# Performance work log

Measured on AMD Instinct MI355X. Metric: run time of the kernel, lower is better.

Reference implementation:

```python
import jax, jax.numpy as jnp
import numpy as np

B, T, E, H = 4, 8192, 1024, 16
D = E // H
SCALE = 1.0 / np.sqrt(D).astype(np.float32)
EPS_FM = 1e-6
EPS_Z = 1e-8


def setup_inputs() -> dict:
    key = jax.random.key(0)
    ks = jax.random.split(key, 11)
    s = 1.0 / np.sqrt(E).astype(np.float32)  # small init so feature map stays sane
    return {
        'query': jax.random.normal(ks[0], (B, T, E), jnp.float32),
        'key': jax.random.normal(ks[1], (B, T, E), jnp.float32),
        'value': jax.random.normal(ks[2], (B, T, E), jnp.float32),
        'Wq': jax.random.normal(ks[3], (E, E), jnp.float32) * s,
        'bq': jax.random.normal(ks[4], (E,), jnp.float32) * 0.01,
        'Wk': jax.random.normal(ks[5], (E, E), jnp.float32) * s,
        'bk': jax.random.normal(ks[6], (E,), jnp.float32) * 0.01,
        'Wv': jax.random.normal(ks[7], (E, E), jnp.float32) * s,
        'bv': jax.random.normal(ks[8], (E,), jnp.float32) * 0.01,
        'Wo': jax.random.normal(ks[9], (E, E), jnp.float32) * s,
        'bo': jax.random.normal(ks[10], (E,), jnp.float32) * 0.01,
    }


def _heads(x):
    # (B, T, E) -> (B, H, T, D)
    b, t, _ = x.shape
    return x.reshape(b, t, H, D).transpose(0, 2, 1, 3)


def _feature_map(x):
    return jax.nn.relu(x) + EPS_FM


def reference(query, key, value, Wq, bq, Wk, bk, Wv, bv, Wo, bo):
    b, tq, _ = query.shape
    Q = _feature_map(_heads(query @ Wq.T + bq) * SCALE)  # (B,H,Tq,D)
    K = _feature_map(_heads(key @ Wk.T + bk) * SCALE)    # (B,H,Tk,D)
    V = _heads(value @ Wv.T + bv)                         # (B,H,Tk,D)
    KV = jnp.einsum('bhnd,bhne->bhde', K, V)              # (B,H,D,D)
    K_sum = K.sum(axis=2)                                 # (B,H,D)
    Z = jnp.einsum('bhnd,bhd->bhn', Q, K_sum) + EPS_Z     # (B,H,Tq)
    out = jnp.einsum('bhnd,bhde->bhne', Q, KV) / Z[..., None]
    out = out.transpose(0, 2, 1, 3).reshape(b, tq, E)
    return out @ Wo.T + bo
```

## Files before the change

kernel.cpp:

```cpp
#include <hip/hip_runtime.h>
#include <hip/hip_bf16.h>


#define SCALE_ 0.125f
#define EPS_FM_ 1e-6f
#define EPS_Z_ 1e-8f

typedef __bf16 bf16;
typedef __attribute__((ext_vector_type(4))) __bf16 bf16x4;
typedef __attribute__((ext_vector_type(8))) __bf16 bf16x8;
typedef __attribute__((ext_vector_type(8))) unsigned short u16x8;
typedef __attribute__((ext_vector_type(4))) float f32x4;

__device__ __forceinline__ void gl_lds16(const void* g, void* l) {
  __builtin_amdgcn_global_load_lds(
      (const __attribute__((address_space(1))) void*)g,
      (__attribute__((address_space(3))) void*)l, 16, 0, 0);
}

#define SBAR()                                  \
  do {                                          \
    __builtin_amdgcn_sched_barrier(0);          \
    asm volatile("s_barrier" ::: "memory");     \
    __builtin_amdgcn_sched_barrier(0);          \
  } while (0)

__global__ __launch_bounds__(256) void cast_weights(
    const float* __restrict__ Wq, const float* __restrict__ Wk,
    const float* __restrict__ Wv, const float* __restrict__ Wo,
    bf16* __restrict__ out) {
  int which = blockIdx.y;
  int j = (blockIdx.x * 256 + threadIdx.x) * 4;
  const float* s = (which == 0) ? Wq : (which == 1) ? Wk : (which == 2) ? Wv : Wo;
  float4 v = *(const float4*)(s + j);
  bf16x4 p = {(bf16)v.x, (bf16)v.y, (bf16)v.z, (bf16)v.w};
  *(bf16x4*)(out + (size_t)which * (1u << 20) + j) = p;
}

template <int OM, int AF>
__global__ __launch_bounds__(512, 2) void gemm8p(
    const bf16* __restrict__ A, const float* __restrict__ Af,
    const bf16* __restrict__ W, const float* __restrict__ bias,
    bf16* __restrict__ Pb, float* __restrict__ Pf) {
  __shared__ __align__(16) char lds[131072];
  const int tid = threadIdx.x;
  const int bid = blockIdx.x;
  const int wg = (bid & 7) * (gridDim.x >> 3) + (bid >> 3);
  const int m0 = (wg >> 2) * 256;
  const int n0 = (wg & 3) * 256;
  const int wave = tid >> 6, lane = tid & 63;
  const int wm = wave >> 2, wn = wave & 3;
  const int l16 = lane & 15, kg = lane >> 4;
  const int e = l16 & 7;
  const int sw0 = (kg ^ e) << 4;
  const int sw1 = ((4 | kg) ^ e) << 4;

  const int tr = tid >> 3;
  const int cslot = (tid & 7) ^ (tr & 7);
  const bf16* pA = nullptr;
  const float* pAf = nullptr;
  if constexpr (AF == 0)
    pA = A + (size_t)(m0 + tr) * 1024 + cslot * 8;
  else
    pAf = Af + (size_t)(m0 + tr) * 1024 + cslot * 8;
  const bf16* pB = W + (size_t)(n0 + ((tr >> 5) << 6) + (tr & 31)) * 1024 + cslot * 8;
  char* sA = lds;
  char* sB = lds + 65536;

  auto stgA = [&](int h, int kt, int bb) {
    const bf16* g = pA + h * 65536 + kt * 64;
    char* d = sA + bb * 32768 + h * 16384 + tid * 16;
    gl_lds16(g, d);
    gl_lds16(g + 131072, d + 8192);
  };
  auto stgB = [&](int h, int kt, int bb) {
    const bf16* g = pB + h * 32768 + kt * 64;
    char* d = sB + bb * 32768 + h * 16384 + tid * 16;
    gl_lds16(g, d);
    gl_lds16(g + 131072, d + 8192);
  };
  auto ldgA = [&](int h, int kt, f32x4* r) {
    const float* g = pAf + h * 65536 + kt * 64;
    r[0] = *(const f32x4*)g;
    r[1] = *(const f32x4*)(g + 4);
    r[2] = *(const f32x4*)(g + 131072);
    r[3] = *(const f32x4*)(g + 131072 + 4);
  };
  auto wrA = [&](int h, int bb, const f32x4* r) {
    bf16x8 p0 = {(bf16)r[0][0], (bf16)r[0][1], (bf16)r[0][2], (bf16)r[0][3],
                 (bf16)r[1][0], (bf16)r[1][1], (bf16)r[1][2], (bf16)r[1][3]};
    bf16x8 p1 = {(bf16)r[2][0], (bf16)r[2][1], (bf16)r[2][2], (bf16)r[2][3],
                 (bf16)r[3][0], (bf16)r[3][1], (bf16)r[3][2], (bf16)r[3][3]};
    char* d = sA + bb * 32768 + h * 16384 + tid * 16;
    *(bf16x8*)d = p0;
    *(bf16x8*)(d + 8192) = p1;
  };

  const int aBase = wm * 8192 + l16 * 128;
  const int bBase = wn * 4096 + l16 * 128;
  auto ldA = [&](int bb, int h, int fmi, int kk) {
    return *(const bf16x8*)(sA + bb * 32768 + h * 16384 + aBase + fmi * 2048 +
                            (kk ? sw1 : sw0));
  };
  auto ldB = [&](int bb, int h, int fnj, int kk) {
    return *(const bf16x8*)(sB + bb * 32768 + h * 16384 + bBase + fnj * 2048 +
                            (kk ? sw1 : sw0));
  };

  f32x4 acc[8][4] = {};
  bf16x8 rA[4][2], rB01[2][2], rB23[2][2];
  f32x4 ga[4], gb[4];
  const int NT = 16;

  if constexpr (AF == 0) {
    stgA(0, 0, 0); stgB(1, 0, 0); stgA(1, 0, 0); stgB(0, 0, 0);
    stgA(0, 1, 1); stgB(1, 1, 1); stgA(1, 1, 1);
    asm volatile("s_waitcnt vmcnt(6)" ::: "memory");
  } else {
    ldgA(0, 0, ga); ldgA(1, 0, gb);
    stgB(1, 0, 0); stgB(0, 0, 0);
    asm volatile("s_waitcnt vmcnt(4)" ::: "memory");
    wrA(0, 0, ga);
    wrA(1, 0, gb);
    ldgA(0, 1, ga); ldgA(1, 1, gb);
    stgB(1, 1, 1);
    asm volatile("s_waitcnt vmcnt(2)" ::: "memory");
    wrA(0, 1, ga);
    wrA(1, 1, gb);
    ldgA(0, 2, ga); ldgA(1, 2, gb);
    asm volatile("s_waitcnt lgkmcnt(0)" ::: "memory");
  }
  SBAR();

#pragma unroll 2
  for (int t = 0; t < NT; ++t) {
    const int c = t & 1;
#pragma unroll
    for (int fmi = 0; fmi < 4; ++fmi) {
      rA[fmi][0] = ldA(c, 0, fmi, 0);
      rA[fmi][1] = ldA(c, 0, fmi, 1);
    }
#pragma unroll
    for (int fnj = 0; fnj < 2; ++fnj) {
      rB01[fnj][0] = ldB(c, 0, fnj, 0);
      rB01[fnj][1] = ldB(c, 0, fnj, 1);
    }
    if (t + 1 < NT) stgB(0, t + 1, c ^ 1);
    SBAR();
    __builtin_amdgcn_s_setprio(1);
#pragma unroll
    for (int fmi = 0; fmi < 4; ++fmi)
#pragma unroll
      for (int fnj = 0; fnj < 2; ++fnj)
#pragma unroll
        for (int kk = 0; kk < 2; ++kk)
          acc[fmi][fnj] = __builtin_amdgcn_mfma_f32_16x16x32_bf16(
              rA[fmi][kk], rB01[fnj][kk], acc[fmi][fnj], 0, 0, 0);
    __builtin_amdgcn_s_setprio(0);
    SBAR();
#pragma unroll
    for (int fnj = 0; fnj < 2; ++fnj) {
      rB23[fnj][0] = ldB(c, 1, fnj, 0);
      rB23[fnj][1] = ldB(c, 1, fnj, 1);
    }
    if constexpr (AF == 0) {
      if (t + 2 < NT) stgA(0, t + 2, c);
    }
    SBAR();
    __builtin_amdgcn_s_setprio(1);
#pragma unroll
    for (int fmi = 0; fmi < 4; ++fmi)
#pragma unroll
      for (int fnj = 0; fnj < 2; ++fnj)
#pragma unroll
        for (int kk = 0; kk < 2; ++kk)
          acc[fmi][2 + fnj] = __builtin_amdgcn_mfma_f32_16x16x32_bf16(
              rA[fmi][kk], rB23[fnj][kk], acc[fmi][2 + fnj], 0, 0, 0);
    __builtin_amdgcn_s_setprio(0);
    SBAR();
    if constexpr (AF == 1) {
      if (t + 2 < NT) {
        wrA(0, c, ga);
        if (t + 3 < NT) ldgA(0, t + 3, ga);
      }
    }
#pragma unroll
    for (int fmi = 0; fmi < 4; ++fmi) {
      rA[fmi][0] = ldA(c, 1, fmi, 0);
      rA[fmi][1] = ldA(c, 1, fmi, 1);
    }
    if (t + 2 < NT) stgB(1, t + 2, c);
    SBAR();
    __builtin_amdgcn_s_setprio(1);
#pragma unroll
    for (int fmi = 0; fmi < 4; ++fmi)
#pragma unroll
      for (int fnj = 0; fnj < 2; ++fnj)
#pragma unroll
        for (int kk = 0; kk < 2; ++kk)
          acc[4 + fmi][2 + fnj] = __builtin_amdgcn_mfma_f32_16x16x32_bf16(
              rA[fmi][kk], rB23[fnj][kk], acc[4 + fmi][2 + fnj], 0, 0, 0);
    __builtin_amdgcn_s_setprio(0);
    SBAR();
    if constexpr (AF == 0) {
      if (t + 2 < NT) {
        stgA(1, t + 2, c);
        asm volatile("s_waitcnt vmcnt(6)" ::: "memory");
      } else {
        asm volatile("s_waitcnt vmcnt(0)" ::: "memory");
      }
    } else {
      if (t + 2 < NT) {
        wrA(1, c, gb);
        if (t + 3 < NT) ldgA(1, t + 3, gb);
      }
      if (t + 3 < NT)
        asm volatile("s_waitcnt vmcnt(10)" ::: "memory");
      else if (t + 2 < NT)
        asm volatile("s_waitcnt vmcnt(2)" ::: "memory");
      else
        asm volatile("s_waitcnt vmcnt(0)" ::: "memory");
    }
    SBAR();
    __builtin_amdgcn_s_setprio(1);
#pragma unroll
    for (int fmi = 0; fmi < 4; ++fmi)
#pragma unroll
      for (int fnj = 0; fnj < 2; ++fnj)
#pragma unroll
        for (int kk = 0; kk < 2; ++kk)
          acc[4 + fmi][fnj] = __builtin_amdgcn_mfma_f32_16x16x32_bf16(
              rA[fmi][kk], rB01[fnj][kk], acc[4 + fmi][fnj], 0, 0, 0);
    __builtin_amdgcn_s_setprio(0);
    SBAR();
  }

#pragma unroll
  for (int fn = 0; fn < 4; ++fn) {
    const int col = n0 + wn * 64 + fn * 16 + l16;
    const float bv = bias[col];
#pragma unroll
    for (int fm = 0; fm < 8; ++fm) {
      const int row = m0 + wm * 128 + fm * 16 + kg * 4;
#pragma unroll
      for (int i = 0; i < 4; ++i) {
        float v = acc[fm][fn][i] + bv;
        if (OM == 0) { v *= SCALE_; v = fmaxf(v, 0.f) + EPS_FM_; }
        if (OM < 2)
          Pb[(size_t)(row + i) * 1024 + col] = (bf16)v;
        else
          Pf[(size_t)(row + i) * 1024 + col] = v;
      }
    }
  }
}

__global__ __launch_bounds__(256) void kv_mfma(
    const bf16* __restrict__ Kp, const bf16* __restrict__ Vp,
    float* __restrict__ KVpart, float* __restrict__ KsumPart) {
  __shared__ __align__(16) char lds[65536];
  char* Kt = lds;
  char* Vt = lds + 32768;
  const int bh = blockIdx.x, split = blockIdx.y;
  const int b = bh >> 4, h = bh & 15;
  const int tid = threadIdx.x;
  const int p = tid >> 3, c = tid & 7;
  const size_t gbase = (size_t)(b * 8192 + split * 256) * 1024 + h * 64 + c * 8;

#pragma unroll
  for (int i = 0; i < 4; ++i) {
    const int t = i * 64 + p * 2;
    const size_t ga = gbase + (size_t)t * 1024;
    bf16x8 k0 = *(const bf16x8*)(Kp + ga);
    bf16x8 k1 = *(const bf16x8*)(Kp + ga + 1024);
    bf16x8 v0 = *(const bf16x8*)(Vp + ga);
    bf16x8 v1 = *(const bf16x8*)(Vp + ga + 1024);
    u16x8 a0 = __builtin_bit_cast(u16x8, k0);
    u16x8 a1 = __builtin_bit_cast(u16x8, k1);
    u16x8 b0 = __builtin_bit_cast(u16x8, v0);
    u16x8 b1 = __builtin_bit_cast(u16x8, v1);
    const int gt = t >> 3, tl = (t & 7) * 2;
#pragma unroll
    for (int j = 0; j < 8; ++j) {
      const int d = c * 8 + j;
      const int off = d * 512 + ((gt ^ (d & 7) ^ c) << 4) + tl;
      *(unsigned int*)(Kt + off) = (unsigned int)a0[j] | ((unsigned int)a1[j] << 16);
      *(unsigned int*)(Vt + off) = (unsigned int)b0[j] | ((unsigned int)b1[j] << 16);
    }
  }
  __syncthreads();

  const int wave = tid >> 6, lane = tid & 63;
  const int wd = wave >> 1, we = wave & 1;
  const int l16 = lane & 15, kg = lane >> 4;
  f32x4 acc[2][2] = {};
  f32x4 accz[2] = {};
  const bf16x8 ones = {1.f, 1.f, 1.f, 1.f, 1.f, 1.f, 1.f, 1.f};

#pragma unroll
  for (int ks = 0; ks < 8; ++ks) {
    const int g = ks * 4 + kg;
    bf16x8 af[2], bf_[2];
#pragma unroll
    for (int f = 0; f < 2; ++f) {
      const int d = wd * 32 + f * 16 + l16;
      af[f] = *(const bf16x8*)(Kt + d * 512 + ((g ^ (d & 7) ^ ((d >> 3) & 7)) << 4));
      const int ee = we * 32 + f * 16 + l16;
      bf_[f] = *(const bf16x8*)(Vt + ee * 512 + ((g ^ (ee & 7) ^ ((ee >> 3) & 7)) << 4));
    }
#pragma unroll
    for (int fa = 0; fa < 2; ++fa) {
#pragma unroll
      for (int fb = 0; fb < 2; ++fb)
        acc[fa][fb] = __builtin_amdgcn_mfma_f32_16x16x32_bf16(
            af[fa], bf_[fb], acc[fa][fb], 0, 0, 0);
      if (we == 0)
        accz[fa] = __builtin_amdgcn_mfma_f32_16x16x32_bf16(
            af[fa], ones, accz[fa], 0, 0, 0);
    }
  }

  float* outp = KVpart + ((size_t)split * 64 + bh) * 4096;
#pragma unroll
  for (int fa = 0; fa < 2; ++fa)
#pragma unroll
    for (int i = 0; i < 4; ++i) {
      const int d = wd * 32 + fa * 16 + kg * 4 + i;
#pragma unroll
      for (int fb = 0; fb < 2; ++fb)
        outp[d * 64 + we * 32 + fb * 16 + l16] = acc[fa][fb][i];
      if (we == 0 && l16 == 0)
        KsumPart[((size_t)split * 64 + bh) * 64 + d] = accz[fa][i];
    }
}

__global__ __launch_bounds__(256) void kv_reduce(
    const float* __restrict__ KVpart, const float* __restrict__ KsumPart,
    bf16* __restrict__ KVt) {
  int bh = blockIdx.x;
  for (int idx = threadIdx.x; idx < 5120; idx += 256) {
    float s = 0.f;
    if (idx < 4096) {
      int e = idx >> 6, d = idx & 63;
      for (int sp = 0; sp < 32; ++sp)
        s += KVpart[((size_t)sp * 64 + bh) * 4096 + d * 64 + e];
    } else if (idx < 4160) {
      int d = idx - 4096;
      for (int sp = 0; sp < 32; ++sp)
        s += KsumPart[((size_t)sp * 64 + bh) * 64 + d];
    }
    KVt[(size_t)bh * 5120 + idx] = (bf16)s;
  }
}

__global__ __launch_bounds__(256) void attn(
    const bf16* __restrict__ KVt, bf16* __restrict__ QA) {
  __shared__ __align__(16) char lds[43008];
  char* Qt = lds;
  char* Bt = lds + 32768;
  const int bh = blockIdx.x, tc = blockIdx.y;
  const int b = bh >> 4, h = bh & 15;
  const int tid = threadIdx.x;
  const int m0 = b * 8192 + tc * 256;

#pragma unroll
  for (int i = 0; i < 8; ++i) {
    const int gidx = i * 256 + tid;
    const int row = gidx >> 3, g = gidx & 7;
    const int gsrc = g ^ (row & 7);
    gl_lds16(QA + (size_t)(m0 + row) * 1024 + h * 64 + gsrc * 8, Qt + gidx * 16);
  }
#pragma unroll
  for (int i = 0; i < 3; ++i) {
    const int gidx = i * 256 + tid;
    if (gidx < 640) {
      const int row = gidx >> 3, g = gidx & 7;
      const int gsrc = g ^ (row & 7);
      gl_lds16(KVt + (size_t)bh * 5120 + row * 64 + gsrc * 8, Bt + gidx * 16);
    }
  }
  __syncthreads();

  const int wave = tid >> 6, lane = tid & 63;
  const int l16 = lane & 15, kg = lane >> 4;
  bf16x8 a[4][2];
#pragma unroll
  for (int fm = 0; fm < 4; ++fm)
#pragma unroll
    for (int kk = 0; kk < 2; ++kk) {
      const int row = wave * 64 + fm * 16 + l16;
      const int g = kk * 4 + kg;
      a[fm][kk] = *(const bf16x8*)(Qt + row * 128 + ((g ^ (row & 7)) << 4));
    }
  f32x4 acc[4][4] = {};
  f32x4 accz[4] = {};
#pragma unroll
  for (int kk = 0; kk < 2; ++kk) {
    const int g = kk * 4 + kg;
    const int zr = 64 + l16;
    bf16x8 bz = *(const bf16x8*)(Bt + zr * 128 + ((g ^ (zr & 7)) << 4));
#pragma unroll
    for (int fn = 0; fn < 4; ++fn) {
      const int br = fn * 16 + l16;
      bf16x8 bb = *(const bf16x8*)(Bt + br * 128 + ((g ^ (br & 7)) << 4));
#pragma unroll
      for (int fm = 0; fm < 4; ++fm)
        acc[fm][fn] = __builtin_amdgcn_mfma_f32_16x16x32_bf16(
            a[fm][kk], bb, acc[fm][fn], 0, 0, 0);
    }
#pragma unroll
    for (int fm = 0; fm < 4; ++fm)
      accz[fm] = __builtin_amdgcn_mfma_f32_16x16x32_bf16(
          a[fm][kk], bz, accz[fm], 0, 0, 0);
  }
  __syncthreads();

#pragma unroll
  for (int fm = 0; fm < 4; ++fm)
#pragma unroll
    for (int i = 0; i < 4; ++i) {
      const float z = __shfl(accz[fm][i], (lane & 48), 64) + EPS_Z_;
      const float rz = 1.0f / z;
      const int row = wave * 64 + fm * 16 + kg * 4 + i;
#pragma unroll
      for (int fn = 0; fn < 4; ++fn) {
        const int col = fn * 16 + l16;
        const int gc = col >> 3;
        bf16 v = (bf16)(acc[fm][fn][i] * rz);
        *(unsigned short*)(Qt + row * 128 + ((gc ^ (row & 7)) << 4) + (col & 7) * 2) =
            __builtin_bit_cast(unsigned short, v);
      }
    }
  __syncthreads();

#pragma unroll
  for (int i = 0; i < 8; ++i) {
    const int gidx = i * 256 + tid;
    const int row = gidx >> 3, g = gidx & 7;
    bf16x8 v = *(const bf16x8*)(Qt + row * 128 + ((g ^ (row & 7)) << 4));
    *(bf16x8*)(QA + (size_t)(m0 + row) * 1024 + h * 64 + g * 8) = v;
  }
}

extern "C" void kernel_launch(void* const* d_in, const int* in_sizes, int n_in,
                              void* d_out, int out_size, void* d_ws, size_t ws_size,
                              hipStream_t stream) {
  const float* query = (const float*)d_in[0];
  const float* key = (const float*)d_in[1];
  const float* value = (const float*)d_in[2];
  const float* Wq = (const float*)d_in[3];
  const float* bq = (const float*)d_in[4];
  const float* Wk = (const float*)d_in[5];
  const float* bk = (const float*)d_in[6];
  const float* Wv = (const float*)d_in[7];
  const float* bv = (const float*)d_in[8];
  const float* Wo = (const float*)d_in[9];
  const float* bo = (const float*)d_in[10];
  float* out = (float*)d_out;

  bf16* ws = (bf16*)d_ws;
  bf16* Wqb = ws;
  bf16* Wkb = ws + (1u << 20);
  bf16* Wvb = ws + (2u << 20);
  bf16* Wob = ws + (3u << 20);
  bf16* Qp = ws + (4u << 20);
  bf16* Kp = Qp + 33554432u;
  bf16* Vp = Kp + 33554432u;
  bf16* KVt = Vp + 33554432u;
  float* KVpart = (float*)d_out + 16777216u;
  float* KsumPart = KVpart + 8388608u;

  cast_weights<<<dim3(1024, 4), 256, 0, stream>>>(Wq, Wk, Wv, Wo, Wqb);

  gemm8p<0, 1><<<512, 512, 0, stream>>>(nullptr, query, Wqb, bq, Qp, nullptr);
  gemm8p<0, 1><<<512, 512, 0, stream>>>(nullptr, key, Wkb, bk, Kp, nullptr);
  gemm8p<1, 1><<<512, 512, 0, stream>>>(nullptr, value, Wvb, bv, Vp, nullptr);

  kv_mfma<<<dim3(64, 32), 256, 0, stream>>>(Kp, Vp, KVpart, KsumPart);
  kv_reduce<<<64, 256, 0, stream>>>(KVpart, KsumPart, KVt);
  attn<<<dim3(64, 32), 256, 0, stream>>>(KVt, Qp);
  gemm8p<2, 0><<<512, 512, 0, stream>>>(Qp, nullptr, Wob, bo, nullptr, out);
}
```

Before: 515.7 us.

## Merge Q/K/V projection GEMMs into one launch and defer fp32 A staging writes

The three input projection GEMMs become a single 1536-block launch. Each block picks its segment (query, key or value), along with the matching weight, bias, output buffer and epilogue mode. Inside the fp32-A path, the LDS writes and next global loads for the A tile now come after the MFMA batch rather than before it, and the vmcnt waits are retuned to match. This is meant to cut launch gaps and tail effects between the three GEMMs and to overlap the A conversion with compute. The cost is a little per-block indexing overhead and a more delicate wait-count schedule.

```diff
diff --git a/kernel.cpp b/kernel.cpp
--- a/kernel.cpp
+++ b/kernel.cpp
@@ -37,16 +37,24 @@
   *(bf16x4*)(out + (size_t)which * (1u << 20) + j) = p;
 }
 
-template <int OM, int AF>
+template <int MODE>
 __global__ __launch_bounds__(512, 2) void gemm8p(
-    const bf16* __restrict__ A, const float* __restrict__ Af,
-    const bf16* __restrict__ W, const float* __restrict__ bias,
+    const bf16* __restrict__ Ab, const float* __restrict__ Aq,
+    const float* __restrict__ Ak, const float* __restrict__ Av,
+    const bf16* __restrict__ Wb, const float* __restrict__ b0,
+    const float* __restrict__ b1, const float* __restrict__ b2,
     bf16* __restrict__ Pb, float* __restrict__ Pf) {
   __shared__ __align__(16) char lds[131072];
   const int tid = threadIdx.x;
   const int bid = blockIdx.x;
   const int wg = (bid & 7) * (gridDim.x >> 3) + (bid >> 3);
-  const int m0 = (wg >> 2) * 256;
+  const int mt = wg >> 2;
+  int seg = 0, om = 2;
+  if constexpr (MODE == 0) {
+    seg = mt >> 7;
+    om = (seg < 2) ? 0 : 1;
+  }
+  const int m0 = (MODE == 0 ? (mt & 127) : mt) * 256;
   const int n0 = (wg & 3) * 256;
   const int wave = tid >> 6, lane = tid & 63;
   const int wm = wave >> 2, wn = wave & 3;
@@ -59,10 +67,14 @@
   const int cslot = (tid & 7) ^ (tr & 7);
   const bf16* pA = nullptr;
   const float* pAf = nullptr;
-  if constexpr (AF == 0)
-    pA = A + (size_t)(m0 + tr) * 1024 + cslot * 8;
-  else
+  if constexpr (MODE == 1)
+    pA = Ab + (size_t)(m0 + tr) * 1024 + cslot * 8;
+  else {
+    const float* Af = (seg == 0) ? Aq : (seg == 1) ? Ak : Av;
     pAf = Af + (size_t)(m0 + tr) * 1024 + cslot * 8;
+  }
+  const bf16* W = (MODE == 0) ? Wb + ((size_t)seg << 20) : Wb;
+  const float* bias = (MODE == 0) ? ((seg == 0) ? b0 : (seg == 1) ? b1 : b2) : b0;
   const bf16* pB = W + (size_t)(n0 + ((tr >> 5) << 6) + (tr & 31)) * 1024 + cslot * 8;
   char* sA = lds;
   char* sB = lds + 65536;
@@ -112,7 +124,7 @@
   f32x4 ga[4], gb[4];
   const int NT = 16;
 
-  if constexpr (AF == 0) {
+  if constexpr (MODE == 1) {
     stgA(0, 0, 0); stgB(1, 0, 0); stgA(1, 0, 0); stgB(0, 0, 0);
     stgA(0, 1, 1); stgB(1, 1, 1); stgA(1, 1, 1);
     asm volatile("s_waitcnt vmcnt(6)" ::: "memory");
@@ -163,7 +175,7 @@
       rB23[fnj][0] = ldB(c, 1, fnj, 0);
       rB23[fnj][1] = ldB(c, 1, fnj, 1);
     }
-    if constexpr (AF == 0) {
+    if constexpr (MODE == 1) {
       if (t + 2 < NT) stgA(0, t + 2, c);
     }
     SBAR();
@@ -178,31 +190,32 @@
               rA[fmi][kk], rB23[fnj][kk], acc[fmi][2 + fnj], 0, 0, 0);
     __builtin_amdgcn_s_setprio(0);
     SBAR();
-    if constexpr (AF == 1) {
+#pragma unroll
+    for (int fmi = 0; fmi < 4; ++fmi) {
+      rA[fmi][0] = ldA(c, 1, fmi, 0);
+      rA[fmi][1] = ldA(c, 1, fmi, 1);
+    }
+    if (t + 2 < NT) stgB(1, t + 2, c);
+    SBAR();
+    __builtin_amdgcn_s_setprio(1);
+#pragma unroll
+    for (int fmi = 0; fmi < 4; ++fmi)
+#pragma unroll
+      for (int fnj = 0; fnj < 2; ++fnj)
+#pragma unroll
+        for (int kk = 0; kk < 2; ++kk)
+          acc[4 + fmi][2 + fnj] = __builtin_amdgcn_mfma_f32_16x16x32_bf16(
+              rA[fmi][kk], rB23[fnj][kk], acc[4 + fmi][2 + fnj], 0, 0, 0);
+    __builtin_amdgcn_s_setprio(0);
+    __builtin_amdgcn_sched_barrier(0);
+    if constexpr (MODE == 0) {
       if (t + 2 < NT) {
         wrA(0, c, ga);
         if (t + 3 < NT) ldgA(0, t + 3, ga);
       }
     }
-#pragma unroll
-    for (int fmi = 0; fmi < 4; ++fmi) {
-      rA[fmi][0] = ldA(c, 1, fmi, 0);
-      rA[fmi][1] = ldA(c, 1, fmi, 1);
-    }
-    if (t + 2 < NT) stgB(1, t + 2, c);
-    SBAR();
-    __builtin_amdgcn_s_setprio(1);
-#pragma unroll
-    for (int fmi = 0; fmi < 4; ++fmi)
-#pragma unroll
-      for (int fnj = 0; fnj < 2; ++fnj)
-#pragma unroll
-        for (int kk = 0; kk < 2; ++kk)
-          acc[4 + fmi][2 + fnj] = __builtin_amdgcn_mfma_f32_16x16x32_bf16(
-              rA[fmi][kk], rB23[fnj][kk], acc[4 + fmi][2 + fnj], 0, 0, 0);
-    __builtin_amdgcn_s_setprio(0);
-    SBAR();
-    if constexpr (AF == 0) {
+    SBAR();
+    if constexpr (MODE == 1) {
       if (t + 2 < NT) {
         stgA(1, t + 2, c);
         asm volatile("s_waitcnt vmcnt(6)" ::: "memory");
@@ -210,31 +223,35 @@
         asm volatile("s_waitcnt vmcnt(0)" ::: "memory");
       }
     } else {
+      if (t + 3 < NT)
+        asm volatile("s_waitcnt vmcnt(6)" ::: "memory");
+      else if (t + 2 < NT)
+        asm volatile("s_waitcnt vmcnt(2)" ::: "memory");
+      else
+        asm volatile("s_waitcnt vmcnt(0)" ::: "memory");
+    }
+    SBAR();
+    __builtin_amdgcn_s_setprio(1);
+#pragma unroll
+    for (int fmi = 0; fmi < 4; ++fmi)
+#pragma unroll
+      for (int fnj = 0; fnj < 2; ++fnj)
+#pragma unroll
+        for (int kk = 0; kk < 2; ++kk)
+          acc[4 + fmi][fnj] = __builtin_amdgcn_mfma_f32_16x16x32_bf16(
+              rA[fmi][kk], rB01[fnj][kk], acc[4 + fmi][fnj], 0, 0, 0);
+    __builtin_amdgcn_s_setprio(0);
+    __builtin_amdgcn_sched_barrier(0);
+    if constexpr (MODE == 0) {
       if (t + 2 < NT) {
         wrA(1, c, gb);
         if (t + 3 < NT) ldgA(1, t + 3, gb);
       }
-      if (t + 3 < NT)
-        asm volatile("s_waitcnt vmcnt(10)" ::: "memory");
-      else if (t + 2 < NT)
-        asm volatile("s_waitcnt vmcnt(2)" ::: "memory");
-      else
-        asm volatile("s_waitcnt vmcnt(0)" ::: "memory");
-    }
-    SBAR();
-    __builtin_amdgcn_s_setprio(1);
-#pragma unroll
-    for (int fmi = 0; fmi < 4; ++fmi)
-#pragma unroll
-      for (int fnj = 0; fnj < 2; ++fnj)
-#pragma unroll
-        for (int kk = 0; kk < 2; ++kk)
-          acc[4 + fmi][fnj] = __builtin_amdgcn_mfma_f32_16x16x32_bf16(
-              rA[fmi][kk], rB01[fnj][kk], acc[4 + fmi][fnj], 0, 0, 0);
-    __builtin_amdgcn_s_setprio(0);
-    SBAR();
-  }
-
+    }
+    SBAR();
+  }
+
+  bf16* PbS = (MODE == 0) ? Pb + (size_t)seg * 33554432u : nullptr;
 #pragma unroll
   for (int fn = 0; fn < 4; ++fn) {
     const int col = n0 + wn * 64 + fn * 16 + l16;
@@ -245,11 +262,12 @@
 #pragma unroll
       for (int i = 0; i < 4; ++i) {
         float v = acc[fm][fn][i] + bv;
-        if (OM == 0) { v *= SCALE_; v = fmaxf(v, 0.f) + EPS_FM_; }
-        if (OM < 2)
-          Pb[(size_t)(row + i) * 1024 + col] = (bf16)v;
-        else
+        if constexpr (MODE == 0) {
+          if (om == 0) { v *= SCALE_; v = fmaxf(v, 0.f) + EPS_FM_; }
+          PbS[(size_t)(row + i) * 1024 + col] = (bf16)v;
+        } else {
           Pf[(size_t)(row + i) * 1024 + col] = v;
+        }
       }
     }
   }
@@ -460,8 +478,6 @@
 
   bf16* ws = (bf16*)d_ws;
   bf16* Wqb = ws;
-  bf16* Wkb = ws + (1u << 20);
-  bf16* Wvb = ws + (2u << 20);
   bf16* Wob = ws + (3u << 20);
   bf16* Qp = ws + (4u << 20);
   bf16* Kp = Qp + 33554432u;
@@ -472,12 +488,12 @@
 
   cast_weights<<<dim3(1024, 4), 256, 0, stream>>>(Wq, Wk, Wv, Wo, Wqb);
 
-  gemm8p<0, 1><<<512, 512, 0, stream>>>(nullptr, query, Wqb, bq, Qp, nullptr);
-  gemm8p<0, 1><<<512, 512, 0, stream>>>(nullptr, key, Wkb, bk, Kp, nullptr);
-  gemm8p<1, 1><<<512, 512, 0, stream>>>(nullptr, value, Wvb, bv, Vp, nullptr);
+  gemm8p<0><<<1536, 512, 0, stream>>>(nullptr, query, key, value, Wqb, bq, bk,
+                                      bv, Qp, nullptr);
 
   kv_mfma<<<dim3(64, 32), 256, 0, stream>>>(Kp, Vp, KVpart, KsumPart);
   kv_reduce<<<64, 256, 0, stream>>>(KVpart, KsumPart, KVt);
   attn<<<dim3(64, 32), 256, 0, stream>>>(KVt, Qp);
-  gemm8p<2, 0><<<512, 512, 0, stream>>>(Qp, nullptr, Wob, bo, nullptr, out);
-}
+  gemm8p<1><<<512, 512, 0, stream>>>(Qp, nullptr, nullptr, nullptr, Wob, bo,
+                                     bo, bo, nullptr, out);
+}
```

After: 514.2 us. Within noise of the previous version (-0.3%).
